# Performance work log

Hardware: AMD Instinct MI355X
Metric: run time of the kernel (lower is better)

Reference implementation:

```python
import jax, jax.numpy as jnp
import numpy as np

T, B, D, H, S = 512, 32, 1024, 1024, 512


def setup_inputs() -> dict:
    key = jax.random.key(0)
    ks = jax.random.split(key, 10)
    sc = 0.02
    return {
        "x": jax.random.normal(ks[0], (T, B, D), jnp.float32),
        "h0": jax.random.normal(ks[1], (B, H), jnp.float32),
        "c0": jax.random.normal(ks[2], (B, H), jnp.float32),
        "ctx": jax.random.normal(ks[3], (S, B, H), jnp.float32),
        # nn.Linear(input_size, 4*hidden_size) with bias
        "W_ih": jax.random.normal(ks[4], (4 * H, D), jnp.float32) * sc,
        "b_ih": jax.random.normal(ks[5], (4 * H,), jnp.float32) * sc,
        # nn.Linear(hidden_size, 4*hidden_size) with bias
        "W_hh": jax.random.normal(ks[6], (4 * H, H), jnp.float32) * sc,
        "b_hh": jax.random.normal(ks[7], (4 * H,), jnp.float32) * sc,
        # SoftDotAttention: linear_in (H->H, no bias), linear_out (2H->H, no bias)
        "W_in": jax.random.normal(ks[8], (H, H), jnp.float32) * sc,
        "W_out": jax.random.normal(ks[9], (H, 2 * H), jnp.float32) * sc,
    }


def reference(x, h0, c0, ctx, W_ih, b_ih, W_hh, b_hh, W_in, W_out):
    ctx_b = jnp.swapaxes(ctx, 0, 1)  # [B, S, H] (ctx.transpose(0,1))

    def step(carry, xt):
        hx, cx = carry
        gates = xt @ W_ih.T + b_ih + hx @ W_hh.T + b_hh  # [B, 4H]
        i, f, g, o = jnp.split(gates, 4, axis=1)
        cy = jax.nn.sigmoid(f) * cx + jax.nn.sigmoid(i) * jnp.tanh(g)
        hy = jax.nn.sigmoid(o) * jnp.tanh(cy)  # [B, H]
        # SoftDotAttention
        target = hy @ W_in.T  # [B, H]
        attn = jax.nn.softmax(jnp.einsum("bsh,bh->bs", ctx_b, target), axis=-1)
        wc = jnp.einsum("bs,bsh->bh", attn, ctx_b)  # weighted context
        h_tilde = jnp.tanh(jnp.concatenate([wc, hy], axis=1) @ W_out.T)
        return (h_tilde, cy), h_tilde

    (hT, cT), out = jax.lax.scan(step, (h0, c0), x)
    return out, hT, cT
```

## Files before the change

kernel.cpp:

```cpp
#include <hip/hip_runtime.h>
#include <hip/hip_bf16.h>
#include <cstdint>
#include <cstddef>

#define TT 512
#define BB 32
#define DD 1024
#define HH 1024
#define SS 512

typedef _Float16 f16x8 __attribute__((ext_vector_type(8)));
typedef _Float16 f16x4 __attribute__((ext_vector_type(4)));
typedef _Float16 f16x2 __attribute__((ext_vector_type(2)));
typedef float f32x4 __attribute__((ext_vector_type(4)));

__device__ __forceinline__ float sigm(float x) { return 1.0f / (1.0f + __expf(-x)); }
__device__ __forceinline__ float tanh_fast(float x) {
    return 1.0f - 2.0f / (__expf(2.0f * x) + 1.0f);
}
__device__ __forceinline__ f16x8 cvt8(const float* __restrict__ p) {
    float4 u = *(const float4*)p;
    float4 v = *(const float4*)(p + 4);
    f16x8 r;
    r[0] = (_Float16)u.x; r[1] = (_Float16)u.y; r[2] = (_Float16)u.z; r[3] = (_Float16)u.w;
    r[4] = (_Float16)v.x; r[5] = (_Float16)v.y; r[6] = (_Float16)v.z; r[7] = (_Float16)v.w;
    return r;
}

__device__ __forceinline__ void st_u32_coh(unsigned* p, unsigned v) {
    __hip_atomic_store(p, v, __ATOMIC_RELAXED, __HIP_MEMORY_SCOPE_AGENT);
}
__device__ __forceinline__ unsigned ld_u32_coh(const unsigned* p) {
    return __hip_atomic_load(p, __ATOMIC_RELAXED, __HIP_MEMORY_SCOPE_AGENT);
}

__global__ __launch_bounds__(256) void k_cvt(const float* __restrict__ s,
                                             _Float16* __restrict__ d, int n4) {
    for (int i = blockIdx.x * blockDim.x + threadIdx.x; i < n4; i += gridDim.x * blockDim.x) {
        float4 v = ((const float4*)s)[i];
        f16x4 h;
        h[0] = (_Float16)v.x; h[1] = (_Float16)v.y;
        h[2] = (_Float16)v.z; h[3] = (_Float16)v.w;
        ((f16x4*)d)[i] = h;
    }
}

__global__ void k_bias(const float* __restrict__ bih, const float* __restrict__ bhh,
                       float* __restrict__ bsum) {
    const int i = blockIdx.x * blockDim.x + threadIdx.x;
    if (i < 4 * HH) bsum[i] = bih[i] + bhh[i];
}

__global__ void k_init(const float* __restrict__ c0, float* __restrict__ cbuf) {
    const int i = blockIdx.x * blockDim.x + threadIdx.x;
    if (i < BB * HH) cbuf[i] = c0[i];
}

__global__ void k_zero(unsigned* __restrict__ p) {
    const int i = blockIdx.x * blockDim.x + threadIdx.x;
    if (i < 1024) p[i] = 0u;
}

__global__ void k_fin(const float* __restrict__ lasth, const float* __restrict__ cbuf,
                      float* __restrict__ hT, float* __restrict__ cT) {
    const int i = blockIdx.x * blockDim.x + threadIdx.x;
    if (i < BB * HH) {
        hT[i] = lasth[i];
        cT[i] = cbuf[i];
    }
}

__global__ __launch_bounds__(256) void k_pre(const float* __restrict__ x,
                                             const float* __restrict__ Wih,
                                             _Float16* __restrict__ gx) {
    const int wave = (blockIdx.x * blockDim.x + threadIdx.x) >> 6;
    const int lane = threadIdx.x & 63;
    const int m0 = (wave >> 6) * 64, n0 = (wave & 63) * 64;
    const int lm = lane & 15, q8 = (lane >> 4) * 8;

    f32x4 acc[4][4];
    #pragma unroll
    for (int i = 0; i < 4; ++i)
        #pragma unroll
        for (int j = 0; j < 4; ++j) acc[i][j] = (f32x4)0.0f;

    for (int k0 = 0; k0 < DD; k0 += 32) {
        f16x8 a[4], b[4];
        #pragma unroll
        for (int i = 0; i < 4; ++i)
            a[i] = cvt8(x + (size_t)(m0 + i * 16 + lm) * DD + k0 + q8);
        #pragma unroll
        for (int j = 0; j < 4; ++j)
            b[j] = cvt8(Wih + (size_t)(n0 + j * 16 + lm) * DD + k0 + q8);
        #pragma unroll
        for (int i = 0; i < 4; ++i)
            #pragma unroll
            for (int j = 0; j < 4; ++j)
                acc[i][j] = __builtin_amdgcn_mfma_f32_16x16x32_f16(a[i], b[j], acc[i][j], 0, 0, 0);
    }
    const int rq = (lane >> 4) * 4;
    #pragma unroll
    for (int i = 0; i < 4; ++i)
        #pragma unroll
        for (int j = 0; j < 4; ++j)
            #pragma unroll
            for (int r = 0; r < 4; ++r)
                gx[(size_t)(m0 + i * 16 + rq + r) * (4 * HH) + n0 + j * 16 + lm] =
                    (_Float16)acc[i][j][r];
}

__global__ __launch_bounds__(256) void k_trwin(const float* __restrict__ Win,
                                               _Float16* __restrict__ WinT) {
    __shared__ float tile[32][33];
    const int bx = blockIdx.x & 31, by = blockIdx.x >> 5;
    const int tx = threadIdx.x & 31, ty = threadIdx.x >> 5;
    #pragma unroll
    for (int r = 0; r < 4; ++r)
        tile[ty + r * 8][tx] = Win[(size_t)(by * 32 + ty + r * 8) * HH + bx * 32 + tx];
    __syncthreads();
    #pragma unroll
    for (int r = 0; r < 4; ++r)
        WinT[(size_t)(bx * 32 + ty + r * 8) * HH + by * 32 + tx] =
            (_Float16)tile[tx][ty + r * 8];
}

__global__ __launch_bounds__(256) void k_ctxw(const float* __restrict__ ctxf,
                                              const _Float16* __restrict__ WinT,
                                              _Float16* __restrict__ ctxW) {
    const int wave = (blockIdx.x * blockDim.x + threadIdx.x) >> 6;
    const int lane = threadIdx.x & 63;
    const int m0 = (wave >> 4) * 64, n0 = (wave & 15) * 64;
    const int lm = lane & 15, q8 = (lane >> 4) * 8;

    f32x4 acc[4][4];
    #pragma unroll
    for (int i = 0; i < 4; ++i)
        #pragma unroll
        for (int j = 0; j < 4; ++j) acc[i][j] = (f32x4)0.0f;

    for (int k0 = 0; k0 < HH; k0 += 32) {
        f16x8 a[4], b[4];
        #pragma unroll
        for (int i = 0; i < 4; ++i)
            a[i] = cvt8(ctxf + (size_t)(m0 + i * 16 + lm) * HH + k0 + q8);
        #pragma unroll
        for (int j = 0; j < 4; ++j)
            b[j] = *(const f16x8*)(WinT + (size_t)(n0 + j * 16 + lm) * HH + k0 + q8);
        #pragma unroll
        for (int i = 0; i < 4; ++i)
            #pragma unroll
            for (int j = 0; j < 4; ++j)
                acc[i][j] = __builtin_amdgcn_mfma_f32_16x16x32_f16(a[i], b[j], acc[i][j], 0, 0, 0);
    }
    const int rq = (lane >> 4) * 4;
    #pragma unroll
    for (int i = 0; i < 4; ++i)
        #pragma unroll
        for (int j = 0; j < 4; ++j)
            #pragma unroll
            for (int r = 0; r < 4; ++r)
                ctxW[(size_t)(m0 + i * 16 + rq + r) * HH + n0 + j * 16 + lm] =
                    (_Float16)acc[i][j][r];
}

__device__ __forceinline__ void gbar5(unsigned* __restrict__ flags, unsigned round) {
    __syncthreads();
    const int tid = threadIdx.x;
    if (tid == 0) {
        asm volatile("s_waitcnt vmcnt(0)" ::: "memory");
        st_u32_coh(&flags[blockIdx.x], round);
    }
    if (tid < 64) {
        int guard = 0;
        for (;;) {
            const unsigned a0 = ld_u32_coh(&flags[tid * 4 + 0]);
            const unsigned a1 = ld_u32_coh(&flags[tid * 4 + 1]);
            const unsigned a2 = ld_u32_coh(&flags[tid * 4 + 2]);
            const unsigned a3 = ld_u32_coh(&flags[tid * 4 + 3]);
            if (a0 >= round && a1 >= round && a2 >= round && a3 >= round) break;
            __builtin_amdgcn_s_sleep(1);
            if (++guard > (1 << 20)) break;
        }
        __builtin_amdgcn_fence(__ATOMIC_ACQUIRE, "agent");
    }
    __syncthreads();
}

__global__ __launch_bounds__(512, 1) void k_persist(
    const _Float16* __restrict__ x16,
    const _Float16* __restrict__ ctx_h,
    const _Float16* __restrict__ ctxW,
    const float* __restrict__ Whh,
    const float* __restrict__ Wih,
    const float* __restrict__ Wout,
    const float* __restrict__ bsum,
    const float* __restrict__ c0i,
    float* __restrict__ cbuf,
    _Float16* __restrict__ h16,
    _Float16* __restrict__ hy16,
    _Float16* __restrict__ wc16,
    float* __restrict__ scores,
    float* __restrict__ out,
    unsigned* __restrict__ bar) {
    __shared__ __align__(16) _Float16 sWHH[16 * 1024];
    __shared__ __align__(16) _Float16 sWIH[16 * 1024];
    __shared__ __align__(16) _Float16 sWOUT[4 * 2048];
    __shared__ __align__(16) float sRED[4096];
    __shared__ float sSM[512];
    __shared__ float sCB[128];

    const int bid = blockIdx.x;
    const int tid = threadIdx.x;
    const int w = tid >> 6, lane = tid & 63;
    const int lm = lane & 15, q8 = (lane >> 4) * 8;
    const int j0 = bid * 4;

    for (int idx = tid; idx < 16 * 128; idx += 512) {
        const int p = idx >> 7, k8 = idx & 127;
        const int g = (p >> 2) * HH + j0 + (p & 3);
        const int dst = (p * 2048 + k8 * 16) ^ ((p & 7) << 4);
        *(f16x8*)((char*)sWHH + dst) = cvt8(Whh + (size_t)g * HH + k8 * 8);
        *(f16x8*)((char*)sWIH + dst) = cvt8(Wih + (size_t)g * DD + k8 * 8);
    }
    for (int idx = tid; idx < 4 * 256; idx += 512) {
        const int p = idx >> 8, k8 = idx & 255;
        *(f16x8*)((char*)sWOUT + ((p * 4096 + k8 * 16) ^ (p << 4))) =
            cvt8(Wout + (size_t)(j0 + p) * (2 * HH) + k8 * 8);
    }
    if (tid < 128) sCB[tid] = c0i[(size_t)(tid >> 2) * HH + j0 + (tid & 3)];
    __syncthreads();

    unsigned round = 0;
    for (int t = 0; t < TT; ++t) {
        {
            const int kb = (w & 3) * 256;
            f32x4 acc0 = (f32x4)0.0f, acc1 = (f32x4)0.0f;
            if (w < 4) {
                #pragma unroll
                for (int kk = 0; kk < 256; kk += 32) {
                    const int k0 = kb + kk + q8;
                    f16x8 a0 = *(const f16x8*)(h16 + (size_t)lm * HH + k0);
                    f16x8 a1 = *(const f16x8*)(h16 + (size_t)(16 + lm) * HH + k0);
                    f16x8 bb = *(const f16x8*)((const char*)sWHH +
                                 ((lm * 2048 + k0 * 2) ^ ((lm & 7) << 4)));
                    acc0 = __builtin_amdgcn_mfma_f32_16x16x32_f16(a0, bb, acc0, 0, 0, 0);
                    acc1 = __builtin_amdgcn_mfma_f32_16x16x32_f16(a1, bb, acc1, 0, 0, 0);
                }
            } else {
                const _Float16* Xb = x16 + (size_t)t * (BB * DD);
                #pragma unroll
                for (int kk = 0; kk < 256; kk += 32) {
                    const int k0 = kb + kk + q8;
                    f16x8 a0 = *(const f16x8*)(Xb + (size_t)lm * DD + k0);
                    f16x8 a1 = *(const f16x8*)(Xb + (size_t)(16 + lm) * DD + k0);
                    f16x8 bb = *(const f16x8*)((const char*)sWIH +
                                 ((lm * 2048 + k0 * 2) ^ ((lm & 7) << 4)));
                    acc0 = __builtin_amdgcn_mfma_f32_16x16x32_f16(a0, bb, acc0, 0, 0, 0);
                    acc1 = __builtin_amdgcn_mfma_f32_16x16x32_f16(a1, bb, acc1, 0, 0, 0);
                }
            }
            ((f32x4*)sRED)[(w * 2 + 0) * 64 + lane] = acc0;
            ((f32x4*)sRED)[(w * 2 + 1) * 64 + lane] = acc1;
            __syncthreads();
            {
                const int b = tid >> 4, p = tid & 15;
                const int mt = b >> 4, bi = b & 15;
                const int ln = ((bi >> 2) << 4) | p, r = bi & 3;
                float gv = 0.0f;
                #pragma unroll
                for (int w2 = 0; w2 < 8; ++w2)
                    gv += sRED[((w2 * 2 + mt) * 64 + ln) * 4 + r];
                sSM[tid] = gv;
            }
            __syncthreads();
            if (tid < 64) {
                const int b = tid >> 1, cp = (tid & 1) * 2;
                union { _Float16 h[2]; unsigned u; } pk;
                #pragma unroll
                for (int cc = 0; cc < 2; ++cc) {
                    const int c = cp + cc, j = j0 + c;
                    const float gi = sSM[b * 16 + 0 + c] + bsum[j];
                    const float gf = sSM[b * 16 + 4 + c] + bsum[HH + j];
                    const float gg = sSM[b * 16 + 8 + c] + bsum[2 * HH + j];
                    const float go = sSM[b * 16 + 12 + c] + bsum[3 * HH + j];
                    const float cprev = sCB[b * 4 + c];
                    const float cy = sigm(gf) * cprev + sigm(gi) * tanh_fast(gg);
                    const float hv = sigm(go) * tanh_fast(cy);
                    sCB[b * 4 + c] = cy;
                    pk.h[cc] = (_Float16)hv;
                }
                st_u32_coh((unsigned*)(hy16 + (size_t)b * HH + j0 + cp), pk.u);
            }
        }
        ++round;
        gbar5(bar, round);

        {
            const int b = bid & 31, s0 = (bid >> 5) * 64;
            const _Float16* hrow = hy16 + (size_t)b * HH + lane * 16;
            const f16x8 hv0 = *(const f16x8*)(hrow);
            const f16x8 hv1 = *(const f16x8*)(hrow + 8);
            float hf[16];
            #pragma unroll
            for (int i = 0; i < 8; ++i) { hf[i] = (float)hv0[i]; hf[8 + i] = (float)hv1[i]; }
            f16x8 cr0[8], cr1[8];
            #pragma unroll
            for (int i = 0; i < 8; ++i) {
                const _Float16* crow =
                    ctxW + ((size_t)(s0 + w * 8 + i) * BB + b) * HH + lane * 16;
                cr0[i] = *(const f16x8*)(crow);
                cr1[i] = *(const f16x8*)(crow + 8);
            }
            #pragma unroll
            for (int i = 0; i < 8; ++i) {
                float sum = 0.0f;
                #pragma unroll
                for (int jj = 0; jj < 8; ++jj)
                    sum += hf[jj] * (float)cr0[i][jj] + hf[8 + jj] * (float)cr1[i][jj];
                #pragma unroll
                for (int off = 32; off > 0; off >>= 1) sum += __shfl_down(sum, off, 64);
                if (lane == 0)
                    st_u32_coh((unsigned*)(scores + b * SS + s0 + w * 8 + i),
                               __float_as_uint(sum));
            }
        }
        ++round;
        gbar5(bar, round);

        {
            const int b = bid >> 3, h0 = (bid & 7) * 128;
            const float v = scores[b * SS + tid];
            float mx = v;
            #pragma unroll
            for (int off = 32; off > 0; off >>= 1) mx = fmaxf(mx, __shfl_xor(mx, off, 64));
            if (lane == 0) sRED[w] = mx;
            __syncthreads();
            mx = sRED[0];
            #pragma unroll
            for (int w2 = 1; w2 < 8; ++w2) mx = fmaxf(mx, sRED[w2]);
            const float e = __expf(v - mx);
            sSM[tid] = e;
            float ssum = e;
            #pragma unroll
            for (int off = 32; off > 0; off >>= 1) ssum += __shfl_xor(ssum, off, 64);
            if (lane == 0) sRED[8 + w] = ssum;
            __syncthreads();
            float tot = 0.0f;
            #pragma unroll
            for (int w2 = 0; w2 < 8; ++w2) tot += sRED[8 + w2];
            const float inv = 1.0f / tot;
            const int g = lane >> 4, c = lane & 15;
            float acc[8];
            #pragma unroll
            for (int j = 0; j < 8; ++j) acc[j] = 0.0f;
            const _Float16* cb =
                ctx_h + ((size_t)(w * 64 + g) * BB + b) * HH + h0 + c * 8;
            #pragma unroll
            for (int i = 0; i < 16; ++i) {
                const float aw = sSM[w * 64 + g + i * 4];
                const f16x8 u = *(const f16x8*)(cb + (size_t)(i * 4) * (BB * HH));
                #pragma unroll
                for (int j = 0; j < 8; ++j) acc[j] += aw * (float)u[j];
            }
            #pragma unroll
            for (int j = 0; j < 8; ++j) {
                acc[j] += __shfl_xor(acc[j], 16, 64);
                acc[j] += __shfl_xor(acc[j], 32, 64);
            }
            __syncthreads();
            if (g == 0) {
                #pragma unroll
                for (int j = 0; j < 8; ++j) sRED[w * 128 + c * 8 + j] = acc[j];
            }
            __syncthreads();
            if (tid < 64) {
                const int cc = tid * 2;
                float sv0 = 0.0f, sv1 = 0.0f;
                #pragma unroll
                for (int w2 = 0; w2 < 8; ++w2) {
                    sv0 += sRED[w2 * 128 + cc];
                    sv1 += sRED[w2 * 128 + cc + 1];
                }
                union { _Float16 h[2]; unsigned u; } pk;
                pk.h[0] = (_Float16)(sv0 * inv);
                pk.h[1] = (_Float16)(sv1 * inv);
                st_u32_coh((unsigned*)(wc16 + (size_t)b * HH + h0 + cc), pk.u);
            }
        }
        ++round;
        gbar5(bar, round);

        {
            const _Float16* Ab = (w < 4) ? wc16 : hy16;
            const int kb = (w & 3) * 256;
            const int koff = (w < 4) ? 0 : HH;
            const int pc = lm & 3;
            f32x4 acc0 = (f32x4)0.0f, acc1 = (f32x4)0.0f;
            #pragma unroll
            for (int kk = 0; kk < 256; kk += 32) {
                const int k0 = kb + kk + q8;
                f16x8 a0 = *(const f16x8*)(Ab + (size_t)lm * HH + k0);
                f16x8 a1 = *(const f16x8*)(Ab + (size_t)(16 + lm) * HH + k0);
                f16x8 bb = *(const f16x8*)((char*)sWOUT +
                             ((pc * 4096 + (koff + k0) * 2) ^ (pc << 4)));
                acc0 = __builtin_amdgcn_mfma_f32_16x16x32_f16(a0, bb, acc0, 0, 0, 0);
                acc1 = __builtin_amdgcn_mfma_f32_16x16x32_f16(a1, bb, acc1, 0, 0, 0);
            }
            ((f32x4*)sRED)[(w * 2 + 0) * 64 + lane] = acc0;
            ((f32x4*)sRED)[(w * 2 + 1) * 64 + lane] = acc1;
            __syncthreads();
            {
                const int b = tid >> 4, p = tid & 15;
                const int mt = b >> 4, bi = b & 15;
                const int ln = ((bi >> 2) << 4) | p, r = bi & 3;
                float v2 = 0.0f;
                #pragma unroll
                for (int w2 = 0; w2 < 8; ++w2)
                    v2 += sRED[((w2 * 2 + mt) * 64 + ln) * 4 + r];
                const float ht = tanh_fast(v2);
                if (p < 4)
                    st_u32_coh((unsigned*)(out + (size_t)t * (BB * HH) + b * HH + j0 + p),
                               __float_as_uint(ht));
                sSM[tid] = ht;
            }
            __syncthreads();
            if (tid < 64) {
                const int b2 = tid >> 1, pp = (tid & 1) * 2;
                union { _Float16 h[2]; unsigned u; } pk;
                pk.h[0] = (_Float16)sSM[b2 * 16 + pp];
                pk.h[1] = (_Float16)sSM[b2 * 16 + pp + 1];
                st_u32_coh((unsigned*)(h16 + (size_t)b2 * HH + j0 + pp), pk.u);
            }
        }
        ++round;
        gbar5(bar, round);
    }

    if (tid < 128)
        st_u32_coh((unsigned*)&cbuf[(size_t)(tid >> 2) * HH + j0 + (tid & 3)],
                   __float_as_uint(sCB[tid]));
}

__global__ __launch_bounds__(64) void k_step1(const float* __restrict__ hprev,
                                              const _Float16* __restrict__ Whh_h,
                                              const float* __restrict__ Whh_f,
                                              const _Float16* __restrict__ gx_t,
                                              const float* __restrict__ xt_f,
                                              const _Float16* __restrict__ Wih_h,
                                              const float* __restrict__ Wih_f,
                                              const float* __restrict__ bsum,
                                              float* __restrict__ cbuf,
                                              float* __restrict__ hy,
                                              int use_pre, int staged) {
    const int wave = blockIdx.x;
    const int lane = threadIdx.x;
    const int m0 = (wave >> 6) * 16;
    const int j0 = (wave & 63) * 16;
    const int lm = lane & 15, q8 = (lane >> 4) * 8;

    f32x4 acc[4];
    #pragma unroll
    for (int q = 0; q < 4; ++q) acc[q] = (f32x4)0.0f;

    const float* arow = hprev + (size_t)(m0 + lm) * HH;
    if (staged) {
        for (int k0 = 0; k0 < HH; k0 += 32) {
            f16x8 a = cvt8(arow + k0 + q8);
            #pragma unroll
            for (int q = 0; q < 4; ++q) {
                f16x8 b = *(const f16x8*)(Whh_h + (size_t)(q * HH + j0 + lm) * HH + k0 + q8);
                acc[q] = __builtin_amdgcn_mfma_f32_16x16x32_f16(a, b, acc[q], 0, 0, 0);
            }
        }
    } else {
        for (int k0 = 0; k0 < HH; k0 += 32) {
            f16x8 a = cvt8(arow + k0 + q8);
            #pragma unroll
            for (int q = 0; q < 4; ++q) {
                f16x8 b = cvt8(Whh_f + (size_t)(q * HH + j0 + lm) * HH + k0 + q8);
                acc[q] = __builtin_amdgcn_mfma_f32_16x16x32_f16(a, b, acc[q], 0, 0, 0);
            }
        }
    }
    if (!use_pre) {
        const float* xrow = xt_f + (size_t)(m0 + lm) * DD;
        if (staged) {
            for (int k0 = 0; k0 < DD; k0 += 32) {
                f16x8 a = cvt8(xrow + k0 + q8);
                #pragma unroll
                for (int q = 0; q < 4; ++q) {
                    f16x8 b = *(const f16x8*)(Wih_h + (size_t)(q * HH + j0 + lm) * DD + k0 + q8);
                    acc[q] = __builtin_amdgcn_mfma_f32_16x16x32_f16(a, b, acc[q], 0, 0, 0);
                }
            }
        } else {
            for (int k0 = 0; k0 < DD; k0 += 32) {
                f16x8 a = cvt8(xrow + k0 + q8);
                #pragma unroll
                for (int q = 0; q < 4; ++q) {
                    f16x8 b = cvt8(Wih_f + (size_t)(q * HH + j0 + lm) * DD + k0 + q8);
                    acc[q] = __builtin_amdgcn_mfma_f32_16x16x32_f16(a, b, acc[q], 0, 0, 0);
                }
            }
        }
    }
    const int rq = (lane >> 4) * 4;
    const int j = j0 + lm;
    const float bs_i = bsum[j], bs_f = bsum[HH + j], bs_g = bsum[2 * HH + j], bs_o = bsum[3 * HH + j];
    #pragma unroll
    for (int r = 0; r < 4; ++r) {
        const int b = m0 + rq + r;
        float gi = acc[0][r] + bs_i, gf = acc[1][r] + bs_f;
        float gg = acc[2][r] + bs_g, go = acc[3][r] + bs_o;
        if (use_pre) {
            const _Float16* g = gx_t + (size_t)b * (4 * HH);
            gi += (float)g[j];
            gf += (float)g[HH + j];
            gg += (float)g[2 * HH + j];
            go += (float)g[3 * HH + j];
        }
        const float cprev = cbuf[b * HH + j];
        const float cy = sigm(gf) * cprev + sigm(gi) * tanh_fast(gg);
        const float hv = sigm(go) * tanh_fast(cy);
        cbuf[b * HH + j] = cy;
        hy[b * HH + j] = hv;
    }
}

__global__ __launch_bounds__(64) void k_target(const float* __restrict__ hy,
                                               const _Float16* __restrict__ Win_h,
                                               const float* __restrict__ Win_f,
                                               float* __restrict__ target,
                                               int staged) {
    const int wave = blockIdx.x;
    const int lane = threadIdx.x;
    const int m0 = (wave >> 6) * 16;
    const int j0 = (wave & 63) * 16;
    const int lm = lane & 15, q8 = (lane >> 4) * 8;

    f32x4 acc = (f32x4)0.0f;
    const float* arow = hy + (size_t)(m0 + lm) * HH;
    if (staged) {
        for (int k0 = 0; k0 < HH; k0 += 32) {
            f16x8 a = cvt8(arow + k0 + q8);
            f16x8 b = *(const f16x8*)(Win_h + (size_t)(j0 + lm) * HH + k0 + q8);
            acc = __builtin_amdgcn_mfma_f32_16x16x32_f16(a, b, acc, 0, 0, 0);
        }
    } else {
        for (int k0 = 0; k0 < HH; k0 += 32) {
            f16x8 a = cvt8(arow + k0 + q8);
            f16x8 b = cvt8(Win_f + (size_t)(j0 + lm) * HH + k0 + q8);
            acc = __builtin_amdgcn_mfma_f32_16x16x32_f16(a, b, acc, 0, 0, 0);
        }
    }
    const int rq = (lane >> 4) * 4;
    const int j = j0 + lm;
    #pragma unroll
    for (int r = 0; r < 4; ++r)
        target[(m0 + rq + r) * HH + j] = acc[r];
}

__global__ __launch_bounds__(256) void k_scores(const _Float16* __restrict__ ctx_h,
                                                const float* __restrict__ ctx_f,
                                                const float* __restrict__ target,
                                                float* __restrict__ scores, int staged) {
    const int idx = (blockIdx.x * blockDim.x + threadIdx.x) >> 6;
    const int lane = threadIdx.x & 63;
    const int b = idx >> 9;
    const int s = idx & 511;
    const float* trow = target + b * HH + lane * 16;
    float4 t0 = *(const float4*)(trow);
    float4 t1 = *(const float4*)(trow + 4);
    float4 t2 = *(const float4*)(trow + 8);
    float4 t3 = *(const float4*)(trow + 12);
    float sum = 0.0f;
    if (staged) {
        const _Float16* crow = ctx_h + ((size_t)s * BB + b) * HH + lane * 16;
        f16x8 c0 = *(const f16x8*)(crow);
        f16x8 c1 = *(const f16x8*)(crow + 8);
        sum += (float)c0[0] * t0.x + (float)c0[1] * t0.y + (float)c0[2] * t0.z + (float)c0[3] * t0.w;
        sum += (float)c0[4] * t1.x + (float)c0[5] * t1.y + (float)c0[6] * t1.z + (float)c0[7] * t1.w;
        sum += (float)c1[0] * t2.x + (float)c1[1] * t2.y + (float)c1[2] * t2.z + (float)c1[3] * t2.w;
        sum += (float)c1[4] * t3.x + (float)c1[5] * t3.y + (float)c1[6] * t3.z + (float)c1[7] * t3.w;
    } else {
        const float* crow = ctx_f + ((size_t)s * BB + b) * HH + lane * 16;
        float4 c0 = *(const float4*)(crow);
        float4 c1 = *(const float4*)(crow + 4);
        float4 c2 = *(const float4*)(crow + 8);
        float4 c3 = *(const float4*)(crow + 12);
        sum += c0.x * t0.x + c0.y * t0.y + c0.z * t0.z + c0.w * t0.w;
        sum += c1.x * t1.x + c1.y * t1.y + c1.z * t1.z + c1.w * t1.w;
        sum += c2.x * t2.x + c2.y * t2.y + c2.z * t2.z + c2.w * t2.w;
        sum += c3.x * t3.x + c3.y * t3.y + c3.z * t3.z + c3.w * t3.w;
    }
    #pragma unroll
    for (int off = 32; off > 0; off >>= 1) sum += __shfl_down(sum, off, 64);
    if (lane == 0) scores[b * SS + s] = sum;
}

__global__ __launch_bounds__(256) void k_attn(const _Float16* __restrict__ ctx_h,
                                              const float* __restrict__ ctx_f,
                                              const float* __restrict__ scores,
                                              float* __restrict__ wc, int staged) {
    __shared__ float sm[SS];
    __shared__ float red[256];
    const int b = blockIdx.x >> 1;
    const int hc = blockIdx.x & 1;
    const int t = threadIdx.x;

    const float v0 = scores[b * SS + t];
    const float v1 = scores[b * SS + 256 + t];
    red[t] = fmaxf(v0, v1);
    __syncthreads();
    for (int o = 128; o > 0; o >>= 1) {
        if (t < o) red[t] = fmaxf(red[t], red[t + o]);
        __syncthreads();
    }
    const float mx = red[0];
    __syncthreads();
    const float e0 = __expf(v0 - mx);
    const float e1 = __expf(v1 - mx);
    sm[t] = e0;
    sm[t + 256] = e1;
    red[t] = e0 + e1;
    __syncthreads();
    for (int o = 128; o > 0; o >>= 1) {
        if (t < o) red[t] += red[t + o];
        __syncthreads();
    }
    const float inv = 1.0f / red[0];

    const int h = hc * 512 + t * 2;
    float a0 = 0.0f, a1 = 0.0f;
    if (staged) {
        const _Float16* cbase = ctx_h + (size_t)b * HH + h;
        #pragma unroll 8
        for (int s = 0; s < SS; ++s) {
            const float a = sm[s];
            const f16x2 u = *(const f16x2*)(cbase + (size_t)s * (BB * HH));
            a0 += a * (float)u[0];
            a1 += a * (float)u[1];
        }
    } else {
        const float* cbase = ctx_f + (size_t)b * HH + h;
        #pragma unroll 8
        for (int s = 0; s < SS; ++s) {
            const float a = sm[s];
            const float2 u = *(const float2*)(cbase + (size_t)s * (BB * HH));
            a0 += a * u.x;
            a1 += a * u.y;
        }
    }
    wc[b * HH + h] = a0 * inv;
    wc[b * HH + h + 1] = a1 * inv;
}

__global__ __launch_bounds__(64) void k_out(const float* __restrict__ wc,
                                            const float* __restrict__ hy,
                                            const _Float16* __restrict__ Wout_h,
                                            const float* __restrict__ Wout_f,
                                            float* __restrict__ out_t,
                                            int staged) {
    const int wave = blockIdx.x;
    const int lane = threadIdx.x;
    const int m0 = (wave >> 6) * 16;
    const int j0 = (wave & 63) * 16;
    const int lm = lane & 15, q8 = (lane >> 4) * 8;

    f32x4 acc = (f32x4)0.0f;
    const float* arow1 = wc + (size_t)(m0 + lm) * HH;
    const float* arow2 = hy + (size_t)(m0 + lm) * HH;
    if (staged) {
        const _Float16* brow = Wout_h + (size_t)(j0 + lm) * (2 * HH);
        for (int k0 = 0; k0 < HH; k0 += 32) {
            f16x8 a = cvt8(arow1 + k0 + q8);
            f16x8 b = *(const f16x8*)(brow + k0 + q8);
            acc = __builtin_amdgcn_mfma_f32_16x16x32_f16(a, b, acc, 0, 0, 0);
        }
        for (int k0 = 0; k0 < HH; k0 += 32) {
            f16x8 a = cvt8(arow2 + k0 + q8);
            f16x8 b = *(const f16x8*)(brow + HH + k0 + q8);
            acc = __builtin_amdgcn_mfma_f32_16x16x32_f16(a, b, acc, 0, 0, 0);
        }
    } else {
        const float* brow = Wout_f + (size_t)(j0 + lm) * (2 * HH);
        for (int k0 = 0; k0 < HH; k0 += 32) {
            f16x8 a = cvt8(arow1 + k0 + q8);
            f16x8 b = cvt8(brow + k0 + q8);
            acc = __builtin_amdgcn_mfma_f32_16x16x32_f16(a, b, acc, 0, 0, 0);
        }
        for (int k0 = 0; k0 < HH; k0 += 32) {
            f16x8 a = cvt8(arow2 + k0 + q8);
            f16x8 b = cvt8(brow + HH + k0 + q8);
            acc = __builtin_amdgcn_mfma_f32_16x16x32_f16(a, b, acc, 0, 0, 0);
        }
    }
    const int rq = (lane >> 4) * 4;
    const int j = j0 + lm;
    #pragma unroll
    for (int r = 0; r < 4; ++r)
        out_t[(m0 + rq + r) * HH + j] = tanh_fast(acc[r]);
}

static constexpr size_t NW_CBUF   = 0;
static constexpr size_t NW_SCORES = 131072;
static constexpr size_t NW_HY16   = 196608;
static constexpr size_t NW_H16    = 262144;
static constexpr size_t NW_WC16   = 327680;
static constexpr size_t NW_BSUM   = 393216;
static constexpr size_t NW_BAR    = 409600;
static constexpr size_t NW_WINT   = 413696;
static constexpr size_t NW_X16    = 2510848;
static constexpr size_t NW_CTXH   = 36065280;
static constexpr size_t NW_CTXW   = 69619712;
static constexpr size_t NW_TOTAL  = 103174144;

extern "C" void kernel_launch(void* const* d_in, const int* in_sizes, int n_in,
                              void* d_out, int out_size, void* d_ws, size_t ws_size,
                              hipStream_t stream) {
    const float* x    = (const float*)d_in[0];
    const float* h0   = (const float*)d_in[1];
    const float* c0   = (const float*)d_in[2];
    const float* ctx  = (const float*)d_in[3];
    const float* Wih  = (const float*)d_in[4];
    const float* bih  = (const float*)d_in[5];
    const float* Whh  = (const float*)d_in[6];
    const float* bhh  = (const float*)d_in[7];
    const float* Win  = (const float*)d_in[8];
    const float* Wout = (const float*)d_in[9];
    float* out = (float*)d_out;
    char* ws = (char*)d_ws;

    if (ws_size >= NW_TOTAL) {
        float* cbuf       = (float*)(ws + NW_CBUF);
        float* scores     = (float*)(ws + NW_SCORES);
        _Float16* hy16    = (_Float16*)(ws + NW_HY16);
        _Float16* h16     = (_Float16*)(ws + NW_H16);
        _Float16* wc16    = (_Float16*)(ws + NW_WC16);
        float* bsum       = (float*)(ws + NW_BSUM);
        unsigned* bar     = (unsigned*)(ws + NW_BAR);
        _Float16* WinT    = (_Float16*)(ws + NW_WINT);
        _Float16* x16     = (_Float16*)(ws + NW_X16);
        _Float16* ctx_h   = (_Float16*)(ws + NW_CTXH);
        _Float16* ctxW    = (_Float16*)(ws + NW_CTXW);

        k_bias<<<16, 256, 0, stream>>>(bih, bhh, bsum);
        k_zero<<<4, 256, 0, stream>>>(bar);
        k_cvt<<<2048, 256, 0, stream>>>(ctx, ctx_h, SS * BB * HH / 4);
        k_cvt<<<4096, 256, 0, stream>>>(x, x16, TT * BB * DD / 4);
        k_cvt<<<32, 256, 0, stream>>>(h0, h16, BB * HH / 4);
        k_trwin<<<1024, 256, 0, stream>>>(Win, WinT);
        k_ctxw<<<1024, 256, 0, stream>>>(ctx, WinT, ctxW);

        k_persist<<<256, 512, 0, stream>>>(x16, ctx_h, ctxW, Whh, Wih, Wout, bsum,
                                           c0, cbuf, h16, hy16, wc16, scores, out, bar);

        float* hT = out + (size_t)TT * BB * HH;
        float* cT = hT + BB * HH;
        k_fin<<<128, 256, 0, stream>>>(out + (size_t)(TT - 1) * BB * HH, cbuf, hT, cT);
        return;
    }

    float* cbuf   = (float*)(ws + 0);
    float* hy     = (float*)(ws + 131072);
    float* target = (float*)(ws + 262144);
    float* scores = (float*)(ws + 393216);
    float* wc     = (float*)(ws + 458752);
    float* bsum   = (float*)(ws + 589824);
    _Float16* Whh_h  = (_Float16*)(ws + 606208);
    _Float16* Win_h  = (_Float16*)(ws + 8994816);
    _Float16* Wout_h = (_Float16*)(ws + 11091968);
    _Float16* Wih_h  = (_Float16*)(ws + 15286272);
    _Float16* ctx_h  = (_Float16*)(ws + 23674880);
    _Float16* gx     = (_Float16*)(ws + 57229312);

    const int staged  = (ws_size >= (size_t)57229312) ? 1 : 0;
    const int use_pre = (ws_size >= (size_t)191447040) ? 1 : 0;

    k_bias<<<16, 256, 0, stream>>>(bih, bhh, bsum);
    k_init<<<128, 256, 0, stream>>>(c0, cbuf);
    if (staged) {
        k_cvt<<<1024, 256, 0, stream>>>(Whh, Whh_h, 4 * HH * HH / 4);
        k_cvt<<<1024, 256, 0, stream>>>(Win, Win_h, HH * HH / 4);
        k_cvt<<<1024, 256, 0, stream>>>(Wout, Wout_h, 2 * HH * HH / 4);
        k_cvt<<<2048, 256, 0, stream>>>(ctx, ctx_h, SS * BB * HH / 4);
        if (!use_pre) k_cvt<<<1024, 256, 0, stream>>>(Wih, Wih_h, 4 * HH * DD / 4);
    }
    if (use_pre) k_pre<<<4096, 256, 0, stream>>>(x, Wih, gx);

    for (int t = 0; t < TT; ++t) {
        const float* hprev = (t == 0) ? h0 : (out + (size_t)(t - 1) * BB * HH);
        const _Float16* gx_t = gx + (size_t)t * BB * 4 * HH;
        const float* xt = x + (size_t)t * BB * DD;
        float* out_t = out + (size_t)t * BB * HH;

        k_step1<<<128, 64, 0, stream>>>(hprev, Whh_h, Whh, gx_t, xt, Wih_h, Wih,
                                        bsum, cbuf, hy, use_pre, staged);
        k_target<<<128, 64, 0, stream>>>(hy, Win_h, Win, target, staged);
        k_scores<<<4096, 256, 0, stream>>>(ctx_h, ctx, target, scores, staged);
        k_attn<<<64, 256, 0, stream>>>(ctx_h, ctx, scores, wc, staged);
        k_out<<<128, 64, 0, stream>>>(wc, hy, Wout_h, Wout, out_t, staged);
    }

    float* hT = out + (size_t)TT * BB * HH;
    float* cT = hT + BB * HH;
    k_fin<<<128, 256, 0, stream>>>(out + (size_t)(TT - 1) * BB * HH, cbuf, hT, cT);
}
```

Before: 23.70 ms.

## Keep ctx slices in registers and repartition output projection per batch row

Each block's per-step ctxW and ctx slices are loaded into registers once before the time loop, so they are no longer re-read from global memory every step. The output projection is repartitioned by batch row, reading a pre-converted fp16 Wout from global memory in place of the shared-memory copy. The acquire fence in the barrier is replaced by coherent atomic loads of shared activations. A per-block rotation of the K loop start is added to spread memory accesses. The register-resident caches add heavy register pressure, and Wout is now streamed from L2 on every step.

```diff
diff --git a/kernel.cpp b/kernel.cpp
--- a/kernel.cpp
+++ b/kernel.cpp
@@ -32,6 +32,15 @@
 }
 __device__ __forceinline__ unsigned ld_u32_coh(const unsigned* p) {
     return __hip_atomic_load(p, __ATOMIC_RELAXED, __HIP_MEMORY_SCOPE_AGENT);
+}
+__device__ __forceinline__ unsigned long long ld_u64_coh(const unsigned long long* p) {
+    return __hip_atomic_load(p, __ATOMIC_RELAXED, __HIP_MEMORY_SCOPE_AGENT);
+}
+__device__ __forceinline__ f16x8 ld16_coh(const _Float16* p) {
+    union { unsigned long long q[2]; f16x8 h; } u;
+    u.q[0] = ld_u64_coh((const unsigned long long*)p);
+    u.q[1] = ld_u64_coh((const unsigned long long*)p + 1);
+    return u.h;
 }
 
 __global__ __launch_bounds__(256) void k_cvt(const float* __restrict__ s,
@@ -163,7 +172,7 @@
                     (_Float16)acc[i][j][r];
 }
 
-__device__ __forceinline__ void gbar5(unsigned* __restrict__ flags, unsigned round) {
+__device__ __forceinline__ void gbar4(unsigned* __restrict__ flags, unsigned round) {
     __syncthreads();
     const int tid = threadIdx.x;
     if (tid == 0) {
@@ -181,7 +190,6 @@
             __builtin_amdgcn_s_sleep(1);
             if (++guard > (1 << 20)) break;
         }
-        __builtin_amdgcn_fence(__ATOMIC_ACQUIRE, "agent");
     }
     __syncthreads();
 }
@@ -192,7 +200,7 @@
     const _Float16* __restrict__ ctxW,
     const float* __restrict__ Whh,
     const float* __restrict__ Wih,
-    const float* __restrict__ Wout,
+    const _Float16* __restrict__ Wout16,
     const float* __restrict__ bsum,
     const float* __restrict__ c0i,
     float* __restrict__ cbuf,
@@ -204,7 +212,6 @@
     unsigned* __restrict__ bar) {
     __shared__ __align__(16) _Float16 sWHH[16 * 1024];
     __shared__ __align__(16) _Float16 sWIH[16 * 1024];
-    __shared__ __align__(16) _Float16 sWOUT[4 * 2048];
     __shared__ __align__(16) float sRED[4096];
     __shared__ float sSM[512];
     __shared__ float sCB[128];
@@ -222,13 +229,30 @@
         *(f16x8*)((char*)sWHH + dst) = cvt8(Whh + (size_t)g * HH + k8 * 8);
         *(f16x8*)((char*)sWIH + dst) = cvt8(Wih + (size_t)g * DD + k8 * 8);
     }
-    for (int idx = tid; idx < 4 * 256; idx += 512) {
-        const int p = idx >> 8, k8 = idx & 255;
-        *(f16x8*)((char*)sWOUT + ((p * 4096 + k8 * 16) ^ (p << 4))) =
-            cvt8(Wout + (size_t)(j0 + p) * (2 * HH) + k8 * 8);
-    }
     if (tid < 128) sCB[tid] = c0i[(size_t)(tid >> 2) * HH + j0 + (tid & 3)];
     __syncthreads();
+
+    const int b2 = bid & 31, s02 = (bid >> 5) * 64;
+    f16x8 cw[16];
+    #pragma unroll
+    for (int i = 0; i < 8; ++i) {
+        const _Float16* crow =
+            ctxW + ((size_t)(s02 + w * 8 + i) * BB + b2) * HH + lane * 16;
+        cw[2 * i] = *(const f16x8*)(crow);
+        cw[2 * i + 1] = *(const f16x8*)(crow + 8);
+    }
+    const int b3 = bid >> 3, h03 = (bid & 7) * 128;
+    const int g3 = lane >> 4, c3 = lane & 15;
+    f16x8 cx[16];
+    {
+        const _Float16* cb =
+            ctx_h + ((size_t)(w * 64 + g3) * BB + b3) * HH + h03 + c3 * 8;
+        #pragma unroll
+        for (int i = 0; i < 16; ++i)
+            cx[i] = *(const f16x8*)(cb + (size_t)(i * 4) * (BB * HH));
+    }
+    const int b4 = bid >> 3, jb4 = (bid & 7) * 128;
+    const int rot = (bid & 7) * 32;
 
     unsigned round = 0;
     for (int t = 0; t < TT; ++t) {
@@ -238,9 +262,9 @@
             if (w < 4) {
                 #pragma unroll
                 for (int kk = 0; kk < 256; kk += 32) {
-                    const int k0 = kb + kk + q8;
-                    f16x8 a0 = *(const f16x8*)(h16 + (size_t)lm * HH + k0);
-                    f16x8 a1 = *(const f16x8*)(h16 + (size_t)(16 + lm) * HH + k0);
+                    const int k0 = kb + ((kk + rot) & 255) + q8;
+                    f16x8 a0 = ld16_coh(h16 + (size_t)lm * HH + k0);
+                    f16x8 a1 = ld16_coh(h16 + (size_t)(16 + lm) * HH + k0);
                     f16x8 bb = *(const f16x8*)((const char*)sWHH +
                                  ((lm * 2048 + k0 * 2) ^ ((lm & 7) << 4)));
                     acc0 = __builtin_amdgcn_mfma_f32_16x16x32_f16(a0, bb, acc0, 0, 0, 0);
@@ -250,7 +274,7 @@
                 const _Float16* Xb = x16 + (size_t)t * (BB * DD);
                 #pragma unroll
                 for (int kk = 0; kk < 256; kk += 32) {
-                    const int k0 = kb + kk + q8;
+                    const int k0 = kb + ((kk + rot) & 255) + q8;
                     f16x8 a0 = *(const f16x8*)(Xb + (size_t)lm * DD + k0);
                     f16x8 a1 = *(const f16x8*)(Xb + (size_t)(16 + lm) * DD + k0);
                     f16x8 bb = *(const f16x8*)((const char*)sWIH +
@@ -293,43 +317,34 @@
             }
         }
         ++round;
-        gbar5(bar, round);
+        gbar4(bar, round);
 
         {
-            const int b = bid & 31, s0 = (bid >> 5) * 64;
-            const _Float16* hrow = hy16 + (size_t)b * HH + lane * 16;
-            const f16x8 hv0 = *(const f16x8*)(hrow);
-            const f16x8 hv1 = *(const f16x8*)(hrow + 8);
+            const _Float16* hrow = hy16 + (size_t)b2 * HH + lane * 16;
+            const f16x8 hv0 = ld16_coh(hrow);
+            const f16x8 hv1 = ld16_coh(hrow + 8);
             float hf[16];
             #pragma unroll
             for (int i = 0; i < 8; ++i) { hf[i] = (float)hv0[i]; hf[8 + i] = (float)hv1[i]; }
-            f16x8 cr0[8], cr1[8];
-            #pragma unroll
-            for (int i = 0; i < 8; ++i) {
-                const _Float16* crow =
-                    ctxW + ((size_t)(s0 + w * 8 + i) * BB + b) * HH + lane * 16;
-                cr0[i] = *(const f16x8*)(crow);
-                cr1[i] = *(const f16x8*)(crow + 8);
-            }
             #pragma unroll
             for (int i = 0; i < 8; ++i) {
                 float sum = 0.0f;
                 #pragma unroll
                 for (int jj = 0; jj < 8; ++jj)
-                    sum += hf[jj] * (float)cr0[i][jj] + hf[8 + jj] * (float)cr1[i][jj];
+                    sum += hf[jj] * (float)cw[2 * i][jj] + hf[8 + jj] * (float)cw[2 * i + 1][jj];
                 #pragma unroll
                 for (int off = 32; off > 0; off >>= 1) sum += __shfl_down(sum, off, 64);
                 if (lane == 0)
-                    st_u32_coh((unsigned*)(scores + b * SS + s0 + w * 8 + i),
+                    st_u32_coh((unsigned*)(scores + b2 * SS + s02 + w * 8 + i),
                                __float_as_uint(sum));
             }
         }
         ++round;
-        gbar5(bar, round);
+        gbar4(bar, round);
 
         {
-            const int b = bid >> 3, h0 = (bid & 7) * 128;
-            const float v = scores[b * SS + tid];
+            const float v =
+                __uint_as_float(ld_u32_coh((const unsigned*)(scores + b3 * SS + tid)));
             float mx = v;
             #pragma unroll
             for (int off = 32; off > 0; off >>= 1) mx = fmaxf(mx, __shfl_xor(mx, off, 64));
@@ -349,91 +364,81 @@
             #pragma unroll
             for (int w2 = 0; w2 < 8; ++w2) tot += sRED[8 + w2];
             const float inv = 1.0f / tot;
-            const int g = lane >> 4, c = lane & 15;
             float acc[8];
             #pragma unroll
-            for (int j = 0; j < 8; ++j) acc[j] = 0.0f;
-            const _Float16* cb =
-                ctx_h + ((size_t)(w * 64 + g) * BB + b) * HH + h0 + c * 8;
+            for (int jj = 0; jj < 8; ++jj) acc[jj] = 0.0f;
             #pragma unroll
             for (int i = 0; i < 16; ++i) {
-                const float aw = sSM[w * 64 + g + i * 4];
-                const f16x8 u = *(const f16x8*)(cb + (size_t)(i * 4) * (BB * HH));
-                #pragma unroll
-                for (int j = 0; j < 8; ++j) acc[j] += aw * (float)u[j];
-            }
-            #pragma unroll
-            for (int j = 0; j < 8; ++j) {
-                acc[j] += __shfl_xor(acc[j], 16, 64);
-                acc[j] += __shfl_xor(acc[j], 32, 64);
+                const float aw = sSM[w * 64 + g3 + i * 4];
+                #pragma unroll
+                for (int jj = 0; jj < 8; ++jj) acc[jj] += aw * (float)cx[i][jj];
+            }
+            #pragma unroll
+            for (int jj = 0; jj < 8; ++jj) {
+                acc[jj] += __shfl_xor(acc[jj], 16, 64);
+                acc[jj] += __shfl_xor(acc[jj], 32, 64);
             }
             __syncthreads();
-            if (g == 0) {
-                #pragma unroll
-                for (int j = 0; j < 8; ++j) sRED[w * 128 + c * 8 + j] = acc[j];
+            if (g3 == 0) {
+                #pragma unroll
+                for (int jj = 0; jj < 8; ++jj) sRED[w * 128 + c3 * 8 + jj] = acc[jj];
             }
             __syncthreads();
             if (tid < 64) {
-                const int cc = tid * 2;
+                const int ccol = tid * 2;
                 float sv0 = 0.0f, sv1 = 0.0f;
                 #pragma unroll
                 for (int w2 = 0; w2 < 8; ++w2) {
-                    sv0 += sRED[w2 * 128 + cc];
-                    sv1 += sRED[w2 * 128 + cc + 1];
+                    sv0 += sRED[w2 * 128 + ccol];
+                    sv1 += sRED[w2 * 128 + ccol + 1];
                 }
                 union { _Float16 h[2]; unsigned u; } pk;
                 pk.h[0] = (_Float16)(sv0 * inv);
                 pk.h[1] = (_Float16)(sv1 * inv);
-                st_u32_coh((unsigned*)(wc16 + (size_t)b * HH + h0 + cc), pk.u);
+                st_u32_coh((unsigned*)(wc16 + (size_t)b3 * HH + h03 + ccol), pk.u);
             }
         }
         ++round;
-        gbar5(bar, round);
+        gbar4(bar, round);
 
         {
-            const _Float16* Ab = (w < 4) ? wc16 : hy16;
-            const int kb = (w & 3) * 256;
-            const int koff = (w < 4) ? 0 : HH;
-            const int pc = lm & 3;
-            f32x4 acc0 = (f32x4)0.0f, acc1 = (f32x4)0.0f;
-            #pragma unroll
-            for (int kk = 0; kk < 256; kk += 32) {
-                const int k0 = kb + kk + q8;
-                f16x8 a0 = *(const f16x8*)(Ab + (size_t)lm * HH + k0);
-                f16x8 a1 = *(const f16x8*)(Ab + (size_t)(16 + lm) * HH + k0);
-                f16x8 bb = *(const f16x8*)((char*)sWOUT +
-                             ((pc * 4096 + (koff + k0) * 2) ^ (pc << 4)));
-                acc0 = __builtin_amdgcn_mfma_f32_16x16x32_f16(a0, bb, acc0, 0, 0, 0);
-                acc1 = __builtin_amdgcn_mfma_f32_16x16x32_f16(a1, bb, acc1, 0, 0, 0);
-            }
-            ((f32x4*)sRED)[(w * 2 + 0) * 64 + lane] = acc0;
-            ((f32x4*)sRED)[(w * 2 + 1) * 64 + lane] = acc1;
+            _Float16* sA = (_Float16*)sRED;
+            if (tid < 256)
+                ((unsigned long long*)sA)[tid] =
+                    ld_u64_coh((const unsigned long long*)(wc16 + (size_t)b4 * HH) + tid);
+            else
+                ((unsigned long long*)sA)[tid] =
+                    ld_u64_coh((const unsigned long long*)(hy16 + (size_t)b4 * HH) +
+                               (tid - 256));
             __syncthreads();
-            {
-                const int b = tid >> 4, p = tid & 15;
-                const int mt = b >> 4, bi = b & 15;
-                const int ln = ((bi >> 2) << 4) | p, r = bi & 3;
-                float v2 = 0.0f;
-                #pragma unroll
-                for (int w2 = 0; w2 < 8; ++w2)
-                    v2 += sRED[((w2 * 2 + mt) * 64 + ln) * 4 + r];
-                const float ht = tanh_fast(v2);
-                if (p < 4)
-                    st_u32_coh((unsigned*)(out + (size_t)t * (BB * HH) + b * HH + j0 + p),
-                               __float_as_uint(ht));
-                sSM[tid] = ht;
-            }
-            __syncthreads();
-            if (tid < 64) {
-                const int b2 = tid >> 1, pp = (tid & 1) * 2;
+            const int jq = tid >> 2, q = tid & 3;
+            const _Float16* wrow = Wout16 + (size_t)(jb4 + jq) * (2 * HH) + q * 512;
+            const _Float16* arow = sA + q * 512;
+            float sum = 0.0f;
+            #pragma unroll 8
+            for (int i = 0; i < 64; ++i) {
+                const f16x8 wv = *(const f16x8*)(wrow + i * 8);
+                const f16x8 av = *(const f16x8*)(arow + i * 8);
+                #pragma unroll
+                for (int jj = 0; jj < 8; ++jj) sum += (float)av[jj] * (float)wv[jj];
+            }
+            sum += __shfl_xor(sum, 1, 64);
+            sum += __shfl_xor(sum, 2, 64);
+            const float ht = tanh_fast(sum);
+            if (q == 0)
+                st_u32_coh(
+                    (unsigned*)(out + (size_t)t * (BB * HH) + (size_t)b4 * HH + jb4 + jq),
+                    __float_as_uint(ht));
+            const float htn = __shfl(ht, (lane + 4) & 63, 64);
+            if ((lane & 7) == 0) {
                 union { _Float16 h[2]; unsigned u; } pk;
-                pk.h[0] = (_Float16)sSM[b2 * 16 + pp];
-                pk.h[1] = (_Float16)sSM[b2 * 16 + pp + 1];
-                st_u32_coh((unsigned*)(h16 + (size_t)b2 * HH + j0 + pp), pk.u);
+                pk.h[0] = (_Float16)ht;
+                pk.h[1] = (_Float16)htn;
+                st_u32_coh((unsigned*)(h16 + (size_t)b4 * HH + jb4 + jq), pk.u);
             }
         }
         ++round;
-        gbar5(bar, round);
+        gbar4(bar, round);
     }
 
     if (tid < 128)
@@ -713,7 +718,8 @@
 static constexpr size_t NW_X16    = 2510848;
 static constexpr size_t NW_CTXH   = 36065280;
 static constexpr size_t NW_CTXW   = 69619712;
-static constexpr size_t NW_TOTAL  = 103174144;
+static constexpr size_t NW_WOUT16 = 103174144;
+static constexpr size_t NW_TOTAL  = 107368448;
 
 extern "C" void kernel_launch(void* const* d_in, const int* in_sizes, int n_in,
                               void* d_out, int out_size, void* d_ws, size_t ws_size,
@@ -743,16 +749,18 @@
         _Float16* x16     = (_Float16*)(ws + NW_X16);
         _Float16* ctx_h   = (_Float16*)(ws + NW_CTXH);
         _Float16* ctxW    = (_Float16*)(ws + NW_CTXW);
+        _Float16* Wout16  = (_Float16*)(ws + NW_WOUT16);
 
         k_bias<<<16, 256, 0, stream>>>(bih, bhh, bsum);
         k_zero<<<4, 256, 0, stream>>>(bar);
         k_cvt<<<2048, 256, 0, stream>>>(ctx, ctx_h, SS * BB * HH / 4);
         k_cvt<<<4096, 256, 0, stream>>>(x, x16, TT * BB * DD / 4);
         k_cvt<<<32, 256, 0, stream>>>(h0, h16, BB * HH / 4);
+        k_cvt<<<512, 256, 0, stream>>>(Wout, Wout16, HH * 2 * HH / 4);
         k_trwin<<<1024, 256, 0, stream>>>(Win, WinT);
         k_ctxw<<<1024, 256, 0, stream>>>(ctx, WinT, ctxW);
 
-        k_persist<<<256, 512, 0, stream>>>(x16, ctx_h, ctxW, Whh, Wih, Wout, bsum,
+        k_persist<<<256, 512, 0, stream>>>(x16, ctx_h, ctxW, Whh, Wih, Wout16, bsum,
                                            c0, cbuf, h16, hy16, wc16, scores, out, bar);
 
         float* hT = out + (size_t)TT * BB * HH;
```

Measured after the change: 41.39 ms. 74.6% more time.

## Stage shared activations in LDS via coherent loads and drop barrier acquire fence

Applied to the files above, without the earlier changes.

Each block now cooperatively loads the full h16, wc16 and hy16 activation matrices into a swizzled LDS buffer using coherent 64-bit atomic loads, then feeds the MFMA loops from LDS instead of reading global memory per wave. The output projection is split into two K phases (wc then hy) with all 8 waves covering 128-wide K slices. The grid barrier's acquire fence is removed, and cross-block reads use coherent loads instead. The sRED buffer is halved, which serialises the reduction into two passes with extra syncthreads. The intent is to cut redundant global/L2 traffic and fence cost, at the price of more block-level syncs and LDS usage.

```diff
diff --git a/kernel.cpp b/kernel.cpp
--- a/kernel.cpp
+++ b/kernel.cpp
@@ -32,6 +32,15 @@
 }
 __device__ __forceinline__ unsigned ld_u32_coh(const unsigned* p) {
     return __hip_atomic_load(p, __ATOMIC_RELAXED, __HIP_MEMORY_SCOPE_AGENT);
+}
+__device__ __forceinline__ unsigned long long ld_u64_coh(const unsigned long long* p) {
+    return __hip_atomic_load(p, __ATOMIC_RELAXED, __HIP_MEMORY_SCOPE_AGENT);
+}
+__device__ __forceinline__ f16x8 ld16_coh(const _Float16* p) {
+    union { unsigned long long q[2]; f16x8 h; } u;
+    u.q[0] = ld_u64_coh((const unsigned long long*)p);
+    u.q[1] = ld_u64_coh((const unsigned long long*)p + 1);
+    return u.h;
 }
 
 __global__ __launch_bounds__(256) void k_cvt(const float* __restrict__ s,
@@ -163,7 +172,7 @@
                     (_Float16)acc[i][j][r];
 }
 
-__device__ __forceinline__ void gbar5(unsigned* __restrict__ flags, unsigned round) {
+__device__ __forceinline__ void gbar4(unsigned* __restrict__ flags, unsigned round) {
     __syncthreads();
     const int tid = threadIdx.x;
     if (tid == 0) {
@@ -181,7 +190,6 @@
             __builtin_amdgcn_s_sleep(1);
             if (++guard > (1 << 20)) break;
         }
-        __builtin_amdgcn_fence(__ATOMIC_ACQUIRE, "agent");
     }
     __syncthreads();
 }
@@ -205,7 +213,8 @@
     __shared__ __align__(16) _Float16 sWHH[16 * 1024];
     __shared__ __align__(16) _Float16 sWIH[16 * 1024];
     __shared__ __align__(16) _Float16 sWOUT[4 * 2048];
-    __shared__ __align__(16) float sRED[4096];
+    __shared__ __align__(16) _Float16 sH[32 * 1024];
+    __shared__ __align__(16) float sRED[2048];
     __shared__ float sSM[512];
     __shared__ float sCB[128];
 
@@ -233,14 +242,24 @@
     unsigned round = 0;
     for (int t = 0; t < TT; ++t) {
         {
+            #pragma unroll
+            for (int u = 0; u < 8; ++u) {
+                const int idx = u * 512 + tid;
+                const int row = idx >> 7, c16 = idx & 127;
+                const f16x8 v = ld16_coh(h16 + (size_t)row * HH + c16 * 8);
+                *(f16x8*)((char*)sH + ((row * 2048 + c16 * 16) ^ ((row & 7) << 4))) = v;
+            }
+            __syncthreads();
             const int kb = (w & 3) * 256;
             f32x4 acc0 = (f32x4)0.0f, acc1 = (f32x4)0.0f;
             if (w < 4) {
                 #pragma unroll
                 for (int kk = 0; kk < 256; kk += 32) {
                     const int k0 = kb + kk + q8;
-                    f16x8 a0 = *(const f16x8*)(h16 + (size_t)lm * HH + k0);
-                    f16x8 a1 = *(const f16x8*)(h16 + (size_t)(16 + lm) * HH + k0);
+                    f16x8 a0 = *(const f16x8*)((const char*)sH +
+                                 ((lm * 2048 + k0 * 2) ^ ((lm & 7) << 4)));
+                    f16x8 a1 = *(const f16x8*)((const char*)sH +
+                                 (((16 + lm) * 2048 + k0 * 2) ^ ((lm & 7) << 4)));
                     f16x8 bb = *(const f16x8*)((const char*)sWHH +
                                  ((lm * 2048 + k0 * 2) ^ ((lm & 7) << 4)));
                     acc0 = __builtin_amdgcn_mfma_f32_16x16x32_f16(a0, bb, acc0, 0, 0, 0);
@@ -259,17 +278,27 @@
                     acc1 = __builtin_amdgcn_mfma_f32_16x16x32_f16(a1, bb, acc1, 0, 0, 0);
                 }
             }
-            ((f32x4*)sRED)[(w * 2 + 0) * 64 + lane] = acc0;
-            ((f32x4*)sRED)[(w * 2 + 1) * 64 + lane] = acc1;
-            __syncthreads();
-            {
+            ((f32x4*)sRED)[w * 64 + lane] = acc0;
+            __syncthreads();
+            if (tid < 256) {
                 const int b = tid >> 4, p = tid & 15;
-                const int mt = b >> 4, bi = b & 15;
+                const int bi = b & 15;
                 const int ln = ((bi >> 2) << 4) | p, r = bi & 3;
                 float gv = 0.0f;
                 #pragma unroll
-                for (int w2 = 0; w2 < 8; ++w2)
-                    gv += sRED[((w2 * 2 + mt) * 64 + ln) * 4 + r];
+                for (int w2 = 0; w2 < 8; ++w2) gv += sRED[(w2 * 64 + ln) * 4 + r];
+                sSM[tid] = gv;
+            }
+            __syncthreads();
+            ((f32x4*)sRED)[w * 64 + lane] = acc1;
+            __syncthreads();
+            if (tid >= 256) {
+                const int b = tid >> 4, p = tid & 15;
+                const int bi = b & 15;
+                const int ln = ((bi >> 2) << 4) | p, r = bi & 3;
+                float gv = 0.0f;
+                #pragma unroll
+                for (int w2 = 0; w2 < 8; ++w2) gv += sRED[(w2 * 64 + ln) * 4 + r];
                 sSM[tid] = gv;
             }
             __syncthreads();
@@ -293,13 +322,13 @@
             }
         }
         ++round;
-        gbar5(bar, round);
+        gbar4(bar, round);
 
         {
             const int b = bid & 31, s0 = (bid >> 5) * 64;
             const _Float16* hrow = hy16 + (size_t)b * HH + lane * 16;
-            const f16x8 hv0 = *(const f16x8*)(hrow);
-            const f16x8 hv1 = *(const f16x8*)(hrow + 8);
+            const f16x8 hv0 = ld16_coh(hrow);
+            const f16x8 hv1 = ld16_coh(hrow + 8);
             float hf[16];
             #pragma unroll
             for (int i = 0; i < 8; ++i) { hf[i] = (float)hv0[i]; hf[8 + i] = (float)hv1[i]; }
@@ -325,11 +354,12 @@
             }
         }
         ++round;
-        gbar5(bar, round);
+        gbar4(bar, round);
 
         {
             const int b = bid >> 3, h0 = (bid & 7) * 128;
-            const float v = scores[b * SS + tid];
+            const float v =
+                __uint_as_float(ld_u32_coh((const unsigned*)(scores + b * SS + tid)));
             float mx = v;
             #pragma unroll
             for (int off = 32; off > 0; off >>= 1) mx = fmaxf(mx, __shfl_xor(mx, off, 64));
@@ -352,7 +382,7 @@
             const int g = lane >> 4, c = lane & 15;
             float acc[8];
             #pragma unroll
-            for (int j = 0; j < 8; ++j) acc[j] = 0.0f;
+            for (int jj = 0; jj < 8; ++jj) acc[jj] = 0.0f;
             const _Float16* cb =
                 ctx_h + ((size_t)(w * 64 + g) * BB + b) * HH + h0 + c * 8;
             #pragma unroll
@@ -360,63 +390,106 @@
                 const float aw = sSM[w * 64 + g + i * 4];
                 const f16x8 u = *(const f16x8*)(cb + (size_t)(i * 4) * (BB * HH));
                 #pragma unroll
-                for (int j = 0; j < 8; ++j) acc[j] += aw * (float)u[j];
-            }
-            #pragma unroll
-            for (int j = 0; j < 8; ++j) {
-                acc[j] += __shfl_xor(acc[j], 16, 64);
-                acc[j] += __shfl_xor(acc[j], 32, 64);
+                for (int jj = 0; jj < 8; ++jj) acc[jj] += aw * (float)u[jj];
+            }
+            #pragma unroll
+            for (int jj = 0; jj < 8; ++jj) {
+                acc[jj] += __shfl_xor(acc[jj], 16, 64);
+                acc[jj] += __shfl_xor(acc[jj], 32, 64);
             }
             __syncthreads();
             if (g == 0) {
                 #pragma unroll
-                for (int j = 0; j < 8; ++j) sRED[w * 128 + c * 8 + j] = acc[j];
+                for (int jj = 0; jj < 8; ++jj) sRED[w * 128 + c * 8 + jj] = acc[jj];
             }
             __syncthreads();
             if (tid < 64) {
-                const int cc = tid * 2;
+                const int ccol = tid * 2;
                 float sv0 = 0.0f, sv1 = 0.0f;
                 #pragma unroll
                 for (int w2 = 0; w2 < 8; ++w2) {
-                    sv0 += sRED[w2 * 128 + cc];
-                    sv1 += sRED[w2 * 128 + cc + 1];
+                    sv0 += sRED[w2 * 128 + ccol];
+                    sv1 += sRED[w2 * 128 + ccol + 1];
                 }
                 union { _Float16 h[2]; unsigned u; } pk;
                 pk.h[0] = (_Float16)(sv0 * inv);
                 pk.h[1] = (_Float16)(sv1 * inv);
-                st_u32_coh((unsigned*)(wc16 + (size_t)b * HH + h0 + cc), pk.u);
+                st_u32_coh((unsigned*)(wc16 + (size_t)b * HH + h0 + ccol), pk.u);
             }
         }
         ++round;
-        gbar5(bar, round);
+        gbar4(bar, round);
 
         {
-            const _Float16* Ab = (w < 4) ? wc16 : hy16;
-            const int kb = (w & 3) * 256;
-            const int koff = (w < 4) ? 0 : HH;
             const int pc = lm & 3;
+            const int kb = w * 128;
             f32x4 acc0 = (f32x4)0.0f, acc1 = (f32x4)0.0f;
             #pragma unroll
-            for (int kk = 0; kk < 256; kk += 32) {
+            for (int u = 0; u < 8; ++u) {
+                const int idx = u * 512 + tid;
+                const int row = idx >> 7, c16 = idx & 127;
+                const f16x8 v = ld16_coh(wc16 + (size_t)row * HH + c16 * 8);
+                *(f16x8*)((char*)sH + ((row * 2048 + c16 * 16) ^ ((row & 7) << 4))) = v;
+            }
+            __syncthreads();
+            #pragma unroll
+            for (int kk = 0; kk < 128; kk += 32) {
                 const int k0 = kb + kk + q8;
-                f16x8 a0 = *(const f16x8*)(Ab + (size_t)lm * HH + k0);
-                f16x8 a1 = *(const f16x8*)(Ab + (size_t)(16 + lm) * HH + k0);
-                f16x8 bb = *(const f16x8*)((char*)sWOUT +
-                             ((pc * 4096 + (koff + k0) * 2) ^ (pc << 4)));
+                f16x8 a0 = *(const f16x8*)((const char*)sH +
+                             ((lm * 2048 + k0 * 2) ^ ((lm & 7) << 4)));
+                f16x8 a1 = *(const f16x8*)((const char*)sH +
+                             (((16 + lm) * 2048 + k0 * 2) ^ ((lm & 7) << 4)));
+                f16x8 bb = *(const f16x8*)((const char*)sWOUT +
+                             ((pc * 4096 + k0 * 2) ^ (pc << 4)));
                 acc0 = __builtin_amdgcn_mfma_f32_16x16x32_f16(a0, bb, acc0, 0, 0, 0);
                 acc1 = __builtin_amdgcn_mfma_f32_16x16x32_f16(a1, bb, acc1, 0, 0, 0);
             }
-            ((f32x4*)sRED)[(w * 2 + 0) * 64 + lane] = acc0;
-            ((f32x4*)sRED)[(w * 2 + 1) * 64 + lane] = acc1;
-            __syncthreads();
-            {
+            __syncthreads();
+            #pragma unroll
+            for (int u = 0; u < 8; ++u) {
+                const int idx = u * 512 + tid;
+                const int row = idx >> 7, c16 = idx & 127;
+                const f16x8 v = ld16_coh(hy16 + (size_t)row * HH + c16 * 8);
+                *(f16x8*)((char*)sH + ((row * 2048 + c16 * 16) ^ ((row & 7) << 4))) = v;
+            }
+            __syncthreads();
+            #pragma unroll
+            for (int kk = 0; kk < 128; kk += 32) {
+                const int k0 = kb + kk + q8;
+                f16x8 a0 = *(const f16x8*)((const char*)sH +
+                             ((lm * 2048 + k0 * 2) ^ ((lm & 7) << 4)));
+                f16x8 a1 = *(const f16x8*)((const char*)sH +
+                             (((16 + lm) * 2048 + k0 * 2) ^ ((lm & 7) << 4)));
+                f16x8 bb = *(const f16x8*)((const char*)sWOUT +
+                             ((pc * 4096 + (HH + k0) * 2) ^ (pc << 4)));
+                acc0 = __builtin_amdgcn_mfma_f32_16x16x32_f16(a0, bb, acc0, 0, 0, 0);
+                acc1 = __builtin_amdgcn_mfma_f32_16x16x32_f16(a1, bb, acc1, 0, 0, 0);
+            }
+            ((f32x4*)sRED)[w * 64 + lane] = acc0;
+            __syncthreads();
+            if (tid < 256) {
                 const int b = tid >> 4, p = tid & 15;
-                const int mt = b >> 4, bi = b & 15;
+                const int bi = b & 15;
                 const int ln = ((bi >> 2) << 4) | p, r = bi & 3;
                 float v2 = 0.0f;
                 #pragma unroll
-                for (int w2 = 0; w2 < 8; ++w2)
-                    v2 += sRED[((w2 * 2 + mt) * 64 + ln) * 4 + r];
+                for (int w2 = 0; w2 < 8; ++w2) v2 += sRED[(w2 * 64 + ln) * 4 + r];
+                const float ht = tanh_fast(v2);
+                if (p < 4)
+                    st_u32_coh((unsigned*)(out + (size_t)t * (BB * HH) + b * HH + j0 + p),
+                               __float_as_uint(ht));
+                sSM[tid] = ht;
+            }
+            __syncthreads();
+            ((f32x4*)sRED)[w * 64 + lane] = acc1;
+            __syncthreads();
+            if (tid >= 256) {
+                const int b = tid >> 4, p = tid & 15;
+                const int bi = b & 15;
+                const int ln = ((bi >> 2) << 4) | p, r = bi & 3;
+                float v2 = 0.0f;
+                #pragma unroll
+                for (int w2 = 0; w2 < 8; ++w2) v2 += sRED[(w2 * 64 + ln) * 4 + r];
                 const float ht = tanh_fast(v2);
                 if (p < 4)
                     st_u32_coh((unsigned*)(out + (size_t)t * (BB * HH) + b * HH + j0 + p),
@@ -433,7 +506,7 @@
             }
         }
         ++round;
-        gbar5(bar, round);
+        gbar4(bar, round);
     }
 
     if (tid < 128)
```

New measurement: 24.88 ms. +5.0%, slower.
